# Optimization experiments

Hardware: AMD Instinct MI355X
Metric: run time of the kernel (lower is better)

The kernel has to match this reference:

```python
import jax, jax.numpy as jnp
import numpy as np

M, N = 4096, 4096  # placement density grid size (even, as the rfft-based kernel assumes)


def _expk(L):
    # precompute_expk(L): [cos(pi*k/(2L)), sin(pi*k/(2L))] stacked -> [L, 2]
    a = np.pi * np.arange(L) / (2.0 * L)
    return np.stack([np.cos(a), np.sin(a)], axis=-1).astype(np.float32)


def setup_inputs() -> dict:
    key = jax.random.key(0)
    x = jax.random.normal(key, (M, N), dtype=jnp.float32)
    return {
        "x": x,
        "expkM": jnp.asarray(_expk(M)),
        "expkN": jnp.asarray(_expk(N)),
    }


def _idct1d(x, expk):
    # Unnormalized IDCT (DCT-III with DC weight 1) along the last axis:
    #   y_u = sum_k x_k * cos(pi*k*(2u+1)/(2L))
    # Makhoul FFT trick: c_k = x_k * exp(i*pi*k/(2L)); v = L*ifft(c);
    #   y[2m] = Re(v[m]),  y[2m+1] = Re(v[L-1-m])
    L = x.shape[-1]
    ek = expk[:, 0] + 1j * expk[:, 1]            # exp(i*pi*k/(2L)), [L]
    v = (jnp.fft.ifft(x * ek, axis=-1) * L).real  # [..., L]
    half = L // 2
    even = v[..., :half]                          # y[0], y[2], ...
    odd = v[..., ::-1][..., :half]                # y[1], y[3], ... (= v[L-1], v[L-2], ...)
    return jnp.stack([even, odd], axis=-1).reshape(x.shape)


def reference(x, expkM, expkN):
    # out[u,v] = sum_{p,q} x[p,q] cos(pi*p*(2u+1)/(2M)) cos(pi*q*(2v+1)/(2N))
    t = _idct1d(x, expkN)                               # transform along N (last dim)
    out = _idct1d(t.swapaxes(-1, -2), expkM)            # transform along M
    return out.swapaxes(-1, -2)
```

## Files before the change

### kernel.cpp

```cpp
#include <hip/hip_runtime.h>
#include <stdint.h>

typedef __bf16 bf16x8_t __attribute__((ext_vector_type(8)));
typedef float f32x4_t __attribute__((ext_vector_type(4)));

__device__ __forceinline__ uint32_t f32_to_bf16_bits(float f) {
    union { float f; uint32_t u; } v; v.f = f;
    return (v.u + 0x7FFFu + ((v.u >> 16) & 1u)) >> 16;
}

__global__ void prep_kernel(const float* __restrict__ X,
                            unsigned short* __restrict__ Ae,
                            unsigned short* __restrict__ Ao,
                            unsigned short* __restrict__ Xe,
                            unsigned short* __restrict__ Xo) {
    if (blockIdx.x < 4096) {
        const int idx = blockIdx.x * 256 + threadIdx.x;
        const int sel = idx >> 19;
        const int e   = idx & ((1 << 19) - 1);
        const int n   = e >> 8;
        const int c0  = (e & 255) << 3;
        const uint32_t tn = (uint32_t)(2 * n + 1);
        unsigned short* dst = sel ? Ao : Ae;
        uint32_t packed[4];
#pragma unroll
        for (int jj = 0; jj < 4; ++jj) {
            uint32_t cA = (uint32_t)(c0 + 2 * jj);
            uint32_t cB = cA + 1;
            uint32_t r0 = ((2u * cA + (uint32_t)sel) * tn) & 16383u;
            uint32_t r1 = ((2u * cB + (uint32_t)sel) * tn) & 16383u;
            float v0 = __cosf((float)r0 * 3.8349519697141e-4f);
            float v1 = __cosf((float)r1 * 3.8349519697141e-4f);
            packed[jj] = f32_to_bf16_bits(v0) | (f32_to_bf16_bits(v1) << 16);
        }
        *(uint4*)(dst + (size_t)n * 2048 + c0) = make_uint4(packed[0], packed[1], packed[2], packed[3]);
    } else {
        const int idx = (blockIdx.x - 4096) * 256 + threadIdx.x;
        const int q   = idx >> 9;
        const int p0  = (idx & 511) << 3;
        const float4* src = (const float4*)(X + (size_t)q * 4096 + p0);
        float4 a = src[0];
        float4 b = src[1];
        uint2 ev, od;
        ev.x = f32_to_bf16_bits(a.x) | (f32_to_bf16_bits(a.z) << 16);
        ev.y = f32_to_bf16_bits(b.x) | (f32_to_bf16_bits(b.z) << 16);
        od.x = f32_to_bf16_bits(a.y) | (f32_to_bf16_bits(a.w) << 16);
        od.y = f32_to_bf16_bits(b.y) | (f32_to_bf16_bits(b.w) << 16);
        *(uint2*)(Xe + (size_t)q * 2048 + (p0 >> 1)) = ev;
        *(uint2*)(Xo + (size_t)q * 2048 + (p0 >> 1)) = od;
    }
}

template <int STAGE>
__global__ __launch_bounds__(256, 2)
void gemm_fused_kernel(const unsigned short* __restrict__ Ae,
                       const unsigned short* __restrict__ Ao,
                       const unsigned short* __restrict__ Re,
                       const unsigned short* __restrict__ Ro,
                       unsigned short* __restrict__ Te,
                       unsigned short* __restrict__ To,
                       float* __restrict__ out) {
    constexpr int KD = 2048;
    constexpr int BK = 64;
    __shared__ __attribute__((aligned(16))) unsigned short lAe[128 * BK];
    __shared__ __attribute__((aligned(16))) unsigned short lAo[128 * BK];
    __shared__ __attribute__((aligned(16))) unsigned short lBe[128 * BK];
    __shared__ __attribute__((aligned(16))) unsigned short lBo[128 * BK];

    const int tid  = threadIdx.x;
    const int wave = tid >> 6;
    const int lane = tid & 63;

    const int tile_m = blockIdx.y << 7;
    const int tile_c = blockIdx.x << 7;

    f32x4_t acc_e[4][4], acc_o[4][4];
#pragma unroll
    for (int i = 0; i < 4; ++i)
#pragma unroll
        for (int j = 0; j < 4; ++j) {
            acc_e[i][j] = (f32x4_t){0.f, 0.f, 0.f, 0.f};
            acc_o[i][j] = (f32x4_t){0.f, 0.f, 0.f, 0.f};
        }

    const int c_base = wave << 6;
    size_t roff[4];
#pragma unroll
    for (int t = 0; t < 4; ++t) {
        const int cl   = c_base + lane + 256 * t;
        const int row  = cl >> 3;
        const int grp  = (cl & 7) ^ (row & 7);
        roff[t] = (size_t)row * KD + ((size_t)grp << 3);
    }

    const unsigned short* gAe = Ae + (size_t)tile_m * KD;
    const unsigned short* gAo = Ao + (size_t)tile_m * KD;
    const unsigned short* gBe = Re + (size_t)tile_c * KD;
    const unsigned short* gBo = Ro + (size_t)tile_c * KD;

    int lbase[4];
#pragma unroll
    for (int t = 0; t < 4; ++t) lbase[t] = (c_base + 256 * t) << 3;

    const int frow = lane & 15;
    const int sw   = frow & 7;
    const int gq   = lane >> 4;
    const int aRowB = ((wave >> 1) * 64 + frow) * BK;
    const int bRowB = ((wave & 1) * 64 + frow) * BK;

#define GLL(gp, lp) __builtin_amdgcn_global_load_lds( \
        (const __attribute__((address_space(1))) uint32_t*)(gp), \
        (__attribute__((address_space(3))) uint32_t*)(lp), 16, 0, 0)

    for (int kt = 0; kt < KD / BK; ++kt) {
        const size_t kadv = (size_t)kt * BK;
        __syncthreads();
#pragma unroll
        for (int t = 0; t < 4; ++t) {
            GLL(gAe + kadv + roff[t], &lAe[lbase[t]]);
            GLL(gAo + kadv + roff[t], &lAo[lbase[t]]);
            GLL(gBe + kadv + roff[t], &lBe[lbase[t]]);
            GLL(gBo + kadv + roff[t], &lBo[lbase[t]]);
        }
        __syncthreads();

#pragma unroll
        for (int kh = 0; kh < 2; ++kh) {
            const int slotOff = (((kh * 4 + gq) ^ sw) << 3);
            {
                bf16x8_t af[4], bfr[4];
#pragma unroll
                for (int i = 0; i < 4; ++i) af[i]  = *(const bf16x8_t*)(&lAe[aRowB + i * 16 * BK + slotOff]);
#pragma unroll
                for (int j = 0; j < 4; ++j) bfr[j] = *(const bf16x8_t*)(&lBe[bRowB + j * 16 * BK + slotOff]);
#pragma unroll
                for (int i = 0; i < 4; ++i)
#pragma unroll
                    for (int j = 0; j < 4; ++j)
                        acc_e[i][j] = __builtin_amdgcn_mfma_f32_16x16x32_bf16(af[i], bfr[j], acc_e[i][j], 0, 0, 0);
            }
            {
                bf16x8_t af[4], bfr[4];
#pragma unroll
                for (int i = 0; i < 4; ++i) af[i]  = *(const bf16x8_t*)(&lAo[aRowB + i * 16 * BK + slotOff]);
#pragma unroll
                for (int j = 0; j < 4; ++j) bfr[j] = *(const bf16x8_t*)(&lBo[bRowB + j * 16 * BK + slotOff]);
#pragma unroll
                for (int i = 0; i < 4; ++i)
#pragma unroll
                    for (int j = 0; j < 4; ++j)
                        acc_o[i][j] = __builtin_amdgcn_mfma_f32_16x16x32_bf16(af[i], bfr[j], acc_o[i][j], 0, 0, 0);
            }
        }
    }
#undef GLL

    const int orow = tile_m + (wave >> 1) * 64 + ((lane >> 4) << 2);
    const int ocol = tile_c + (wave & 1) * 64 + (lane & 15);
    if (STAGE == 1) {
        unsigned short* dst = (ocol & 1) ? To : Te;
#pragma unroll
        for (int i = 0; i < 4; ++i)
#pragma unroll
            for (int j = 0; j < 4; ++j)
#pragma unroll
                for (int r = 0; r < 4; ++r) {
                    const int n = orow + i * 16 + r;
                    const int c = (ocol + j * 16) >> 1;
                    const float e = acc_e[i][j][r], o = acc_o[i][j][r];
                    dst[(size_t)n * 2048 + c]          = (unsigned short)f32_to_bf16_bits(e + o);
                    dst[(size_t)(4095 - n) * 2048 + c] = (unsigned short)f32_to_bf16_bits(e - o);
                }
    } else {
#pragma unroll
        for (int i = 0; i < 4; ++i)
#pragma unroll
            for (int j = 0; j < 4; ++j)
#pragma unroll
                for (int r = 0; r < 4; ++r) {
                    const int m = orow + i * 16 + r;
                    const int w = ocol + j * 16;
                    const float e = acc_e[i][j][r], o = acc_o[i][j][r];
                    out[(size_t)m * 4096 + w]          = e + o;
                    out[(size_t)(4095 - m) * 4096 + w] = e - o;
                }
    }
}

extern "C" void kernel_launch(void* const* d_in, const int* in_sizes, int n_in,
                              void* d_out, int out_size, void* d_ws, size_t ws_size,
                              hipStream_t stream) {
    const float* x = (const float*)d_in[0];
    char* ws = (char*)d_ws;
    const size_t MB = 1024 * 1024;
    unsigned short* Ae = (unsigned short*)(ws);
    unsigned short* Ao = (unsigned short*)(ws + 8 * MB);
    unsigned short* Xe = (unsigned short*)(ws + 16 * MB);
    unsigned short* Xo = (unsigned short*)(ws + 32 * MB);
    unsigned short* Te = (unsigned short*)(ws + 48 * MB);
    unsigned short* To = (unsigned short*)(ws + 64 * MB);
    float* out = (float*)d_out;

    prep_kernel<<<12288, 256, 0, stream>>>(x, Ae, Ao, Xe, Xo);

    dim3 grid(32, 16);
    gemm_fused_kernel<1><<<grid, 256, 0, stream>>>(Ae, Ao, Xe, Xo, Te, To, nullptr);
    gemm_fused_kernel<2><<<grid, 256, 0, stream>>>(Ae, Ao, Te, To, nullptr, nullptr, out);
}
```

Baseline: 255.4 us.

## Double-buffer LDS tiles with BK=32 to overlap global loads with MFMA

Halves the K tile to 32 and splits each LDS operand into two buffers, so the global-to-LDS loads for the next K slice are issued before computing on the current one. The swizzle pattern is changed to fit the 4-group row layout. This aims to hide global load latency behind MFMA work. In exchange it keeps the same LDS footprint, uses one barrier per smaller step, and relies on the barrier placement being correct so that async global_load_lds writes are complete before they are read.

Measured after the change: 283.3 us. 10.9% more time.

```diff
diff --git a/kernel.cpp b/kernel.cpp
--- a/kernel.cpp
+++ b/kernel.cpp
@@ -61,11 +61,15 @@
                        unsigned short* __restrict__ To,
                        float* __restrict__ out) {
     constexpr int KD = 2048;
-    constexpr int BK = 64;
-    __shared__ __attribute__((aligned(16))) unsigned short lAe[128 * BK];
-    __shared__ __attribute__((aligned(16))) unsigned short lAo[128 * BK];
-    __shared__ __attribute__((aligned(16))) unsigned short lBe[128 * BK];
-    __shared__ __attribute__((aligned(16))) unsigned short lBo[128 * BK];
+    constexpr int BK = 32;
+    __shared__ __attribute__((aligned(16))) unsigned short lAe0[128 * BK];
+    __shared__ __attribute__((aligned(16))) unsigned short lAe1[128 * BK];
+    __shared__ __attribute__((aligned(16))) unsigned short lAo0[128 * BK];
+    __shared__ __attribute__((aligned(16))) unsigned short lAo1[128 * BK];
+    __shared__ __attribute__((aligned(16))) unsigned short lBe0[128 * BK];
+    __shared__ __attribute__((aligned(16))) unsigned short lBe1[128 * BK];
+    __shared__ __attribute__((aligned(16))) unsigned short lBo0[128 * BK];
+    __shared__ __attribute__((aligned(16))) unsigned short lBo1[128 * BK];
 
     const int tid  = threadIdx.x;
     const int wave = tid >> 6;
@@ -84,13 +88,15 @@
         }
 
     const int c_base = wave << 6;
-    size_t roff[4];
-#pragma unroll
-    for (int t = 0; t < 4; ++t) {
-        const int cl   = c_base + lane + 256 * t;
-        const int row  = cl >> 3;
-        const int grp  = (cl & 7) ^ (row & 7);
-        roff[t] = (size_t)row * KD + ((size_t)grp << 3);
+    size_t roff[2];
+    int lbase[2];
+#pragma unroll
+    for (int t = 0; t < 2; ++t) {
+        const int cl  = c_base + lane + 256 * t;
+        const int row = cl >> 2;
+        const int grp = (cl & 3) ^ ((cl >> 3) & 3);
+        roff[t]  = (size_t)row * KD + ((size_t)grp << 3);
+        lbase[t] = (c_base + 256 * t) << 3;
     }
 
     const unsigned short* gAe = Ae + (size_t)tile_m * KD;
@@ -98,13 +104,10 @@
     const unsigned short* gBe = Re + (size_t)tile_c * KD;
     const unsigned short* gBo = Ro + (size_t)tile_c * KD;
 
-    int lbase[4];
-#pragma unroll
-    for (int t = 0; t < 4; ++t) lbase[t] = (c_base + 256 * t) << 3;
-
     const int frow = lane & 15;
-    const int sw   = frow & 7;
+    const int swz  = (frow >> 1) & 3;
     const int gq   = lane >> 4;
+    const int slotOff = ((gq ^ swz) << 3);
     const int aRowB = ((wave >> 1) * 64 + frow) * BK;
     const int bRowB = ((wave & 1) * 64 + frow) * BK;
 
@@ -112,47 +115,53 @@
         (const __attribute__((address_space(1))) uint32_t*)(gp), \
         (__attribute__((address_space(3))) uint32_t*)(lp), 16, 0, 0)
 
-    for (int kt = 0; kt < KD / BK; ++kt) {
-        const size_t kadv = (size_t)kt * BK;
+#define STAGE_TO(lae, lao, lbe, lbo) do { \
+    _Pragma("unroll") \
+    for (int t = 0; t < 2; ++t) { \
+        GLL(gAe + roff[t], &lae[lbase[t]]); \
+        GLL(gAo + roff[t], &lao[lbase[t]]); \
+        GLL(gBe + roff[t], &lbe[lbase[t]]); \
+        GLL(gBo + roff[t], &lbo[lbase[t]]); \
+    } \
+    gAe += BK; gAo += BK; gBe += BK; gBo += BK; \
+} while (0)
+
+#define COMPUTE(lae, lao, lbe, lbo) do { \
+    bf16x8_t af[4], bfr[4]; \
+    _Pragma("unroll") \
+    for (int i = 0; i < 4; ++i) af[i]  = *(const bf16x8_t*)(&lae[aRowB + i * 16 * BK + slotOff]); \
+    _Pragma("unroll") \
+    for (int j = 0; j < 4; ++j) bfr[j] = *(const bf16x8_t*)(&lbe[bRowB + j * 16 * BK + slotOff]); \
+    _Pragma("unroll") \
+    for (int i = 0; i < 4; ++i) \
+        _Pragma("unroll") \
+        for (int j = 0; j < 4; ++j) \
+            acc_e[i][j] = __builtin_amdgcn_mfma_f32_16x16x32_bf16(af[i], bfr[j], acc_e[i][j], 0, 0, 0); \
+    _Pragma("unroll") \
+    for (int i = 0; i < 4; ++i) af[i]  = *(const bf16x8_t*)(&lao[aRowB + i * 16 * BK + slotOff]); \
+    _Pragma("unroll") \
+    for (int j = 0; j < 4; ++j) bfr[j] = *(const bf16x8_t*)(&lbo[bRowB + j * 16 * BK + slotOff]); \
+    _Pragma("unroll") \
+    for (int i = 0; i < 4; ++i) \
+        _Pragma("unroll") \
+        for (int j = 0; j < 4; ++j) \
+            acc_o[i][j] = __builtin_amdgcn_mfma_f32_16x16x32_bf16(af[i], bfr[j], acc_o[i][j], 0, 0, 0); \
+} while (0)
+
+    STAGE_TO(lAe0, lAo0, lBe0, lBo0);
+
+    for (int kt2 = 0; kt2 < 32; ++kt2) {
         __syncthreads();
-#pragma unroll
-        for (int t = 0; t < 4; ++t) {
-            GLL(gAe + kadv + roff[t], &lAe[lbase[t]]);
-            GLL(gAo + kadv + roff[t], &lAo[lbase[t]]);
-            GLL(gBe + kadv + roff[t], &lBe[lbase[t]]);
-            GLL(gBo + kadv + roff[t], &lBo[lbase[t]]);
-        }
+        STAGE_TO(lAe1, lAo1, lBe1, lBo1);
+        COMPUTE(lAe0, lAo0, lBe0, lBo0);
+
         __syncthreads();
-
-#pragma unroll
-        for (int kh = 0; kh < 2; ++kh) {
-            const int slotOff = (((kh * 4 + gq) ^ sw) << 3);
-            {
-                bf16x8_t af[4], bfr[4];
-#pragma unroll
-                for (int i = 0; i < 4; ++i) af[i]  = *(const bf16x8_t*)(&lAe[aRowB + i * 16 * BK + slotOff]);
-#pragma unroll
-                for (int j = 0; j < 4; ++j) bfr[j] = *(const bf16x8_t*)(&lBe[bRowB + j * 16 * BK + slotOff]);
-#pragma unroll
-                for (int i = 0; i < 4; ++i)
-#pragma unroll
-                    for (int j = 0; j < 4; ++j)
-                        acc_e[i][j] = __builtin_amdgcn_mfma_f32_16x16x32_bf16(af[i], bfr[j], acc_e[i][j], 0, 0, 0);
-            }
-            {
-                bf16x8_t af[4], bfr[4];
-#pragma unroll
-                for (int i = 0; i < 4; ++i) af[i]  = *(const bf16x8_t*)(&lAo[aRowB + i * 16 * BK + slotOff]);
-#pragma unroll
-                for (int j = 0; j < 4; ++j) bfr[j] = *(const bf16x8_t*)(&lBo[bRowB + j * 16 * BK + slotOff]);
-#pragma unroll
-                for (int i = 0; i < 4; ++i)
-#pragma unroll
-                    for (int j = 0; j < 4; ++j)
-                        acc_o[i][j] = __builtin_amdgcn_mfma_f32_16x16x32_bf16(af[i], bfr[j], acc_o[i][j], 0, 0, 0);
-            }
-        }
-    }
+        if (kt2 != 31)
+            STAGE_TO(lAe0, lAo0, lBe0, lBo0);
+        COMPUTE(lAe1, lAo1, lBe1, lBo1);
+    }
+#undef COMPUTE
+#undef STAGE_TO
 #undef GLL
 
     const int orow = tile_m + (wave >> 1) * 64 + ((lane >> 4) << 2);
```
